# Kernel optimization log

Measured on AMD Instinct MI355X. Metric: run time of the kernel, lower is better.

Reference implementation:

```python
import jax, jax.numpy as jnp
import numpy as np

B, C, H, W = 4, 96, 56, 56
K0, K1, DIL, HID = 5, 7, 3, 4  # HID: ConvMlp(dim, expansion, drop) => hidden_features = int(mlp_ratio) = 4 (repo quirk)
EPS = 1e-5


def _conv(x, w, b, pad, dil=1, groups=1):
    y = jax.lax.conv_general_dilated(x, w, (1, 1), [(pad, pad), (pad, pad)],
                                     rhs_dilation=(dil, dil),
                                     dimension_numbers=('NCHW', 'OIHW', 'NCHW'),
                                     feature_group_count=groups)
    return y + b[None, :, None, None]


def _conv1x1(x, w, b):
    return jnp.einsum('bchw,oc->bohw', x, w) + b[None, :, None, None]


def _ln(x, g, b):
    # LayerNormProxy: LayerNorm over channel dim of NCHW
    mu = jnp.mean(x, axis=1, keepdims=True)
    v = jnp.var(x, axis=1, keepdims=True)
    return (x - mu) * jax.lax.rsqrt(v + EPS) * g[None, :, None, None] + b[None, :, None, None]


def _gelu(x):
    return jax.nn.gelu(x, approximate=False)  # torch nn.GELU default = exact erf


def _deform_dw(x, ow, ob, dw, db, k, dil, pad):
    # DeformConv2d wrapper: offsets from a same-geometry conv, then depthwise deformable conv.
    Bx, Cx, Hx, Wx = x.shape
    P = k * k
    off = _conv(x, ow, ob, pad, dil).reshape(Bx, P, 2, Hx, Wx)  # [B,P,(y,x),H,W]
    ky = (jnp.repeat(jnp.arange(k), k) * dil - pad).astype(x.dtype)  # row-major kernel grid
    kx = (jnp.tile(jnp.arange(k), k) * dil - pad).astype(x.dtype)
    py = jnp.arange(Hx, dtype=x.dtype)[None, None, :, None] + ky[None, :, None, None] + off[:, :, 0]
    px = jnp.arange(Wx, dtype=x.dtype)[None, None, None, :] + kx[None, :, None, None] + off[:, :, 1]
    y0 = jnp.floor(py)
    x0 = jnp.floor(px)
    wy = py - y0
    wx = px - x0
    xf = x.reshape(Bx, Cx, Hx * Wx)

    def corner(yi, xi):
        valid = (yi >= 0) & (yi < Hx) & (xi >= 0) & (xi < Wx)
        idx = (jnp.clip(yi, 0, Hx - 1).astype(jnp.int32) * Wx
               + jnp.clip(xi, 0, Wx - 1).astype(jnp.int32)).reshape(Bx, -1)
        g = jax.vmap(lambda a, i: jnp.take(a, i, axis=1))(xf, idx).reshape(Bx, Cx, P, Hx, Wx)
        return g * valid[:, None].astype(x.dtype)

    v = (corner(y0, x0) * ((1 - wy) * (1 - wx))[:, None]
         + corner(y0, x0 + 1) * ((1 - wy) * wx)[:, None]
         + corner(y0 + 1, x0) * (wy * (1 - wx))[:, None]
         + corner(y0 + 1, x0 + 1) * (wy * wx)[:, None])  # [B,C,P,H,W]
    return jnp.einsum('bcphw,cp->bchw', v, dw) + db[None, :, None, None]


def setup_inputs() -> dict:
    key = jax.random.key(0)
    ks = iter(jax.random.split(key, 32))

    def rn(shape, s=1.0):
        return jax.random.normal(next(ks), shape, jnp.float32) * s

    f32 = jnp.float32
    return {
        'x': rn((B, C, H, W)),
        'g1n': jnp.ones((C,), f32), 'b1n': jnp.zeros((C,), f32),
        'p1w': rn((C, C), 1 / np.sqrt(C)), 'p1b': jnp.zeros((C,), f32),
        'o0w': rn((2 * K0 * K0, C, K0, K0), 0.05 / np.sqrt(C * K0 * K0)), 'o0b': jnp.zeros((2 * K0 * K0,), f32),
        'd0w': rn((C, K0 * K0), 1 / np.sqrt(K0 * K0)), 'd0b': jnp.zeros((C,), f32),
        'o1w': rn((2 * K1 * K1, C, K1, K1), 0.05 / np.sqrt(C * K1 * K1)), 'o1b': jnp.zeros((2 * K1 * K1,), f32),
        'd1w': rn((C, K1 * K1), 1 / np.sqrt(K1 * K1)), 'd1b': jnp.zeros((C,), f32),
        'c1w': rn((C, C), 1 / np.sqrt(C)), 'c1b': jnp.zeros((C,), f32),
        'p2w': rn((C, C), 1 / np.sqrt(C)), 'p2b': jnp.zeros((C,), f32),
        'ls1': jnp.full((C,), 0.01, f32),
        'g2n': jnp.ones((C,), f32), 'b2n': jnp.zeros((C,), f32),
        'f1w': rn((HID, C), 1 / np.sqrt(C)), 'f1b': jnp.zeros((HID,), f32),
        'dww': rn((HID, 1, 3, 3), 1 / 3.0), 'dwb': jnp.zeros((HID,), f32),
        'f2w': rn((C, HID), 1 / np.sqrt(HID)), 'f2b': jnp.zeros((C,), f32),
        'ls2': jnp.full((C,), 0.01, f32),
    }


def reference(x, g1n, b1n, p1w, p1b, o0w, o0b, d0w, d0b, o1w, o1b, d1w, d1b,
              c1w, c1b, p2w, p2b, ls1, g2n, b2n, f1w, f1b, dww, dwb, f2w, f2b, ls2):
    # attention branch
    y = _ln(x, g1n, b1n)
    shortcut = y
    y = _gelu(_conv1x1(y, p1w, p1b))
    u = y
    a = _deform_dw(y, o0w, o0b, d0w, d0b, K0, 1, K0 // 2)
    a = _deform_dw(a, o1w, o1b, d1w, d1b, K1, DIL, (K1 // 2) * DIL)
    a = _conv1x1(a, c1w, c1b)
    y = _conv1x1(u * a, p2w, p2b) + shortcut
    y = ls1[None, :, None, None] * y
    x = x + y
    # MLP branch (note: norm2 is applied to the branch output y, as in the source)
    z = _ln(y, g2n, b2n)
    z = _conv1x1(z, f1w, f1b)
    z = _gelu(_conv(z, dww, dwb, 1, 1, HID))
    z = _conv1x1(z, f2w, f2b)
    x = x + ls2[None, :, None, None] * z
    return x
```

## Files before the change

kernel.cpp:

```cpp
#include <hip/hip_runtime.h>
#include <math.h>

namespace {

constexpr int Bc = 4, Cc = 96, Hc = 56, Wc = 56;
constexpr int HWc = Hc * Wc;
constexpr int Nc  = Bc * HWc;
constexpr float EPSc = 1e-5f;

typedef __attribute__((ext_vector_type(8))) short bf16x8;
typedef __attribute__((ext_vector_type(4))) float f32x4;
typedef __attribute__((ext_vector_type(4))) unsigned int u32x4;

__device__ __forceinline__ unsigned short f2bf(float f) {
  union { float f; unsigned u; } x; x.f = f;
  unsigned r = x.u + 0x7fffu + ((x.u >> 16) & 1u);
  return (unsigned short)(r >> 16);
}
__device__ __forceinline__ float bf2f(unsigned short u) {
  union { unsigned u; float f; } x; x.u = (unsigned)u << 16; return x.f;
}
__device__ __forceinline__ float gelu_exact(float x) {
  return 0.5f * x * (1.0f + erff(x * 0.7071067811865475f));
}

__global__ __launch_bounds__(256) void k_ln(const float* __restrict__ x,
                                            const float* __restrict__ g,
                                            const float* __restrict__ b,
                                            unsigned short* __restrict__ outN) {
  int pos = blockIdx.x * 256 + threadIdx.x;
  int bb = pos / HWc, hw = pos % HWc;
  const float* xb = x + (size_t)bb * Cc * HWc + hw;
  float s = 0.f, s2 = 0.f;
  for (int c = 0; c < Cc; ++c) { float v = xb[c * HWc]; s += v; s2 += v * v; }
  float mu  = s * (1.f / Cc);
  float var = fmaxf(s2 * (1.f / Cc) - mu * mu, 0.f);
  float rs  = rsqrtf(var + EPSc);
  unsigned short* ob = outN + (size_t)pos * Cc;
  for (int q = 0; q < 12; ++q) {
    unsigned short t8[8];
#pragma unroll
    for (int j = 0; j < 8; ++j) {
      int c = q * 8 + j;
      t8[j] = f2bf((xb[c * HWc] - mu) * rs * g[c] + b[c]);
    }
    *reinterpret_cast<bf16x8*>(ob + q * 8) = *reinterpret_cast<const bf16x8*>(t8);
  }
}

template <int K_, int MTILES, int P>
__global__ __launch_bounds__(256) void k_pack_w(const float* __restrict__ wsrc,
                                                unsigned short* __restrict__ wpk) {
  constexpr int TOTAL = K_ * K_ * 3 * MTILES * 512;
  int idx = blockIdx.x * 256 + threadIdx.x;
  if (idx >= TOTAL) return;
  int j    = idx & 7;
  int lane = (idx >> 3) & 63;
  int t    = idx >> 9;
  int mt   = t % MTILES;
  int step = t / MTILES;
  int o = mt * 16 + (lane & 15);
  int k = step * 32 + ((lane >> 4) & 3) * 8 + j;
  int p = k / Cc, c = k % Cc;
  float v = 0.f;
  if (o < P) v = wsrc[(((size_t)o * Cc + c) * K_ + p / K_) * K_ + (p % K_)];
  wpk[idx] = f2bf(v);
}

__global__ __launch_bounds__(256) void k_pack_dwt(const float* __restrict__ dwsrc,
                                                  float* __restrict__ dwt, int KK) {
  int idx = blockIdx.x * 256 + threadIdx.x;
  if (idx >= KK * Cc) return;
  int p = idx / Cc, c = idx % Cc;
  dwt[idx] = dwsrc[c * KK + p];
}

template <int GELU, int PADP, int WP>
__global__ __launch_bounds__(256) void k_pwg(const unsigned short* __restrict__ inN,
                                             const unsigned short* __restrict__ wpk,
                                             const float* __restrict__ bq,
                                             unsigned short* __restrict__ outPad) {
  int lane = threadIdx.x & 63;
  int wv = threadIdx.x >> 6;
  int ng = wv & 1, mg = wv >> 1;
  int n = blockIdx.x * 32 + ng * 16 + (lane & 15);
  int ko = ((lane >> 4) & 3) * 8;
  const unsigned short* ib = inN + (size_t)n * Cc + ko;
  const unsigned short* wl = wpk + (size_t)lane * 8;
  f32x4 acc[3];
#pragma unroll
  for (int m = 0; m < 3; ++m) acc[m] = (f32x4){0.f, 0.f, 0.f, 0.f};
#pragma unroll
  for (int ks = 0; ks < 3; ++ks) {
    bf16x8 bf = *reinterpret_cast<const bf16x8*>(ib + ks * 32);
#pragma unroll
    for (int m = 0; m < 3; ++m) {
      bf16x8 af = *reinterpret_cast<const bf16x8*>(wl + (size_t)(ks * 6 + mg * 3 + m) * 512);
      acc[m] = __builtin_amdgcn_mfma_f32_16x16x32_bf16(af, bf, acc[m], 0, 0, 0);
    }
  }
  int bb = n / HWc, hw = n % HWc;
  int h = hw / Wc, w = hw % Wc;
  unsigned short* ob = outPad + (((size_t)bb * (Hc + 2 * PADP) + h + PADP) * WP + w + PADP) * Cc;
  int orow = ((lane >> 4) & 3) * 4;
#pragma unroll
  for (int m = 0; m < 3; ++m) {
    int o0 = (mg * 3 + m) * 16 + orow;
    float4 bv = *reinterpret_cast<const float4*>(bq + o0);
    unsigned short t4[4];
#pragma unroll
    for (int j = 0; j < 4; ++j) {
      float r = acc[m][j] + ((const float*)&bv)[j];
      if (GELU) r = gelu_exact(r);
      t4[j] = f2bf(r);
    }
    *reinterpret_cast<uint2*>(ob + o0) = *reinterpret_cast<const uint2*>(t4);
  }
}

template <int UPADP, int UWP>
__global__ __launch_bounds__(256) void k_comb(const unsigned short* __restrict__ uPad,
                                              const unsigned short* __restrict__ An,
                                              const unsigned short* __restrict__ wpk,
                                              const float* __restrict__ bq,
                                              const unsigned short* __restrict__ ylnN,
                                              const float* __restrict__ ls1q,
                                              const float* __restrict__ x,
                                              float* __restrict__ out,
                                              unsigned short* __restrict__ y2N) {
  int lane = threadIdx.x & 63;
  int wv = threadIdx.x >> 6;
  int ng = wv & 1, mg = wv >> 1;
  int n = blockIdx.x * 32 + ng * 16 + (lane & 15);
  int ko = ((lane >> 4) & 3) * 8;
  int bb = n / HWc, hw = n % HWc;
  int h = hw / Wc, w = hw % Wc;
  const unsigned short* ub = uPad + (((size_t)bb * (Hc + 2 * UPADP) + h + UPADP) * UWP + w + UPADP) * Cc + ko;
  const unsigned short* ab = An + (size_t)n * Cc + ko;
  const unsigned short* wl = wpk + (size_t)lane * 8;
  f32x4 acc[3];
#pragma unroll
  for (int m = 0; m < 3; ++m) acc[m] = (f32x4){0.f, 0.f, 0.f, 0.f};
#pragma unroll
  for (int ks = 0; ks < 3; ++ks) {
    bf16x8 uv = *reinterpret_cast<const bf16x8*>(ub + ks * 32);
    bf16x8 av = *reinterpret_cast<const bf16x8*>(ab + ks * 32);
    union { bf16x8 v; unsigned short s[8]; } uu, aa, gg;
    uu.v = uv; aa.v = av;
#pragma unroll
    for (int j = 0; j < 8; ++j) gg.s[j] = f2bf(bf2f(uu.s[j]) * bf2f(aa.s[j]));
#pragma unroll
    for (int m = 0; m < 3; ++m) {
      bf16x8 af = *reinterpret_cast<const bf16x8*>(wl + (size_t)(ks * 6 + mg * 3 + m) * 512);
      acc[m] = __builtin_amdgcn_mfma_f32_16x16x32_bf16(af, gg.v, acc[m], 0, 0, 0);
    }
  }
  int orow = ((lane >> 4) & 3) * 4;
  const float* xb = x + (size_t)bb * Cc * HWc + hw;
  float* ob = out + (size_t)bb * Cc * HWc + hw;
#pragma unroll
  for (int m = 0; m < 3; ++m) {
    int o0 = (mg * 3 + m) * 16 + orow;
    float4 bv = *reinterpret_cast<const float4*>(bq + o0);
    float4 lv = *reinterpret_cast<const float4*>(ls1q + o0);
    uint2 yl = *reinterpret_cast<const uint2*>(ylnN + (size_t)n * Cc + o0);
    unsigned short yl4[4];
    *reinterpret_cast<uint2*>(yl4) = yl;
    unsigned short t4[4];
#pragma unroll
    for (int j = 0; j < 4; ++j) {
      float t = acc[m][j] + ((const float*)&bv)[j] + bf2f(yl4[j]);
      float y2 = ((const float*)&lv)[j] * t;
      t4[j] = f2bf(y2);
      ob[(size_t)(o0 + j) * HWc] = xb[(size_t)(o0 + j) * HWc] + y2;
    }
    *reinterpret_cast<uint2*>(y2N + (size_t)n * Cc + o0) = *reinterpret_cast<const uint2*>(t4);
  }
}

template <int K_, int DIL_, int MTILES, int P, int PADP, int WP, int PSTR, int SPLIT>
__global__ __launch_bounds__(256) void k_conv_mfma(const unsigned short* __restrict__ inp,
                                                   const unsigned short* __restrict__ wpk,
                                                   const float* __restrict__ bq,
                                                   float* __restrict__ dstT) {
  constexpr int KK = K_ * K_;
  constexpr int KKb = KK / SPLIT, KKr = KK % SPLIT;
  constexpr int HP = Hc + 2 * PADP;
  int lane = threadIdx.x & 63;
  int wv = threadIdx.x >> 6;
  int sp = blockIdx.y;
  int p0 = sp * KKb + min(sp, KKr);
  int pcnt = KKb + (sp < KKr ? 1 : 0);
  int n0 = blockIdx.x * 128 + wv * 32 + (lane & 15);
  int n1 = n0 + 16;
  int b0 = n0 / HWc, hw0 = n0 % HWc, h0 = hw0 / Wc, w0 = hw0 % Wc;
  int b1 = n1 / HWc, hw1 = n1 % HWc, h1 = hw1 / Wc, w1 = hw1 % Wc;
  int co = ((lane >> 4) & 3) * 8;
  const unsigned short* ib0 = inp + ((size_t)b0 * HP * WP + (size_t)h0 * WP + w0) * Cc + co;
  const unsigned short* ib1 = inp + ((size_t)b1 * HP * WP + (size_t)h1 * WP + w1) * Cc + co;
  const unsigned short* wl = wpk + (size_t)lane * 8;

  f32x4 acc[MTILES][2];
#pragma unroll
  for (int mt = 0; mt < MTILES; ++mt) {
    acc[mt][0] = (f32x4){0.f, 0.f, 0.f, 0.f};
    acc[mt][1] = (f32x4){0.f, 0.f, 0.f, 0.f};
  }

  for (int pi = 0; pi < pcnt; ++pi) {
    int p = p0 + pi;
    size_t toff = (size_t)((p / K_) * DIL_ * WP + (p % K_) * DIL_) * Cc;
    union { u32x4 u; bf16x8 v; } b0r[3], b1r[3];
#pragma unroll
    for (int cc = 0; cc < 3; ++cc) {
      b0r[cc].u = __builtin_nontemporal_load(reinterpret_cast<const u32x4*>(ib0 + toff + cc * 32));
      b1r[cc].u = __builtin_nontemporal_load(reinterpret_cast<const u32x4*>(ib1 + toff + cc * 32));
    }
#pragma unroll
    for (int cc = 0; cc < 3; ++cc) {
      const unsigned short* wa = wl + (size_t)(p * 3 + cc) * MTILES * 512;
#pragma unroll
      for (int mt = 0; mt < MTILES; ++mt) {
        bf16x8 A = *reinterpret_cast<const bf16x8*>(wa + (size_t)mt * 512);
        acc[mt][0] = __builtin_amdgcn_mfma_f32_16x16x32_bf16(A, b0r[cc].v, acc[mt][0], 0, 0, 0);
        acc[mt][1] = __builtin_amdgcn_mfma_f32_16x16x32_bf16(A, b1r[cc].v, acc[mt][1], 0, 0, 0);
      }
    }
  }

  float* dsp = dstT + (size_t)sp * Nc * PSTR;
  int orow = ((lane >> 4) & 3) * 4;
#pragma unroll
  for (int mt = 0; mt < MTILES; ++mt) {
#pragma unroll
    for (int nt = 0; nt < 2; ++nt) {
      float4 st;
#pragma unroll
      for (int j = 0; j < 4; ++j) {
        int o = mt * 16 + orow + j;
        float bias = (sp == 0 && o < P) ? bq[o] : 0.f;
        ((float*)&st)[j] = acc[mt][nt][j] + bias;
      }
      int n = nt ? n1 : n0;
      *reinterpret_cast<float4*>(dsp + (size_t)n * PSTR + mt * 16 + orow) = st;
    }
  }
}

template <int K_, int DIL_, int PAD_, int PSTR, int NSUM>
__global__ __launch_bounds__(256) void k_meta(const float* __restrict__ offT,
                                              uint4* __restrict__ meta) {
  constexpr int KK = K_ * K_;
  int idx = blockIdx.x * 256 + threadIdx.x;
  if (idx >= Nc * KK) return;
  int p = idx % KK, pos = idx / KK;
  int hw = pos % HWc;
  int h = hw / Wc, w = hw % Wc;
  const float* ob = offT + (size_t)pos * PSTR + 2 * p;
  float oy = ob[0], ox = ob[1];
#pragma unroll
  for (int q = 1; q < NSUM; ++q) {
    oy += ob[(size_t)q * Nc * PSTR];
    ox += ob[(size_t)q * Nc * PSTR + 1];
  }
  float py = (float)(h + (p / K_) * DIL_ - PAD_) + oy;
  float px = (float)(w + (p % K_) * DIL_ - PAD_) + ox;
  float y0f = floorf(py), x0f = floorf(px);
  float wy = py - y0f, wx = px - x0f;
  int y0 = (int)y0f, x0 = (int)x0f;
  int y1 = y0 + 1, x1 = x0 + 1;
  bool y0v = (unsigned)y0 < (unsigned)Hc, y1v = (unsigned)y1 < (unsigned)Hc;
  bool x0v = (unsigned)x0 < (unsigned)Wc, x1v = (unsigned)x1 < (unsigned)Wc;
  int y0c = min(max(y0, 0), Hc - 1), y1c = min(max(y1, 0), Hc - 1);
  int x0c = min(max(x0, 0), Wc - 1), x1c = min(max(x1, 0), Wc - 1);
  float w00 = (y0v && x0v) ? (1.f - wy) * (1.f - wx) : 0.f;
  float w01 = (y0v && x1v) ? (1.f - wy) * wx : 0.f;
  float w10 = (y1v && x0v) ? wy * (1.f - wx) : 0.f;
  float w11 = (y1v && x1v) ? wy * wx : 0.f;
  uint4 m;
  m.x = (unsigned)(y0c | (y1c << 6) | (x0c << 12) | (x1c << 18));
  m.y = 0;
  m.z = (unsigned)f2bf(w00) | ((unsigned)f2bf(w01) << 16);
  m.w = (unsigned)f2bf(w10) | ((unsigned)f2bf(w11) << 16);
  meta[idx] = m;
}

template <int K_, int IPADP, int IWP, int OPADP, int OWP>
__global__ __launch_bounds__(256) void k_deform3(const unsigned short* __restrict__ srcT,
                                                 const uint4* __restrict__ meta,
                                                 const float* __restrict__ dwt,
                                                 const float* __restrict__ dbq,
                                                 unsigned short* __restrict__ dstPad) {
  constexpr int KK = K_ * K_;
  constexpr int IHP = Hc + 2 * IPADP;
  __shared__ float sdwt[KK * Cc];
  for (int i = threadIdx.x; i < KK * Cc; i += 256) sdwt[i] = dwt[i];
  __syncthreads();

  int tid = blockIdx.x * 256 + threadIdx.x;
  int cg = tid % 24;
  int pos = tid / 24;
  int c = cg * 4;
  int bb = pos / HWc, hw = pos % HWc;
  int h = hw / Wc, w = hw % Wc;
  const unsigned short* sb = srcT + ((size_t)bb * IHP * IWP + IPADP * IWP + IPADP) * Cc + c;
  const uint4* mt = meta + (size_t)pos * KK;
  float ac0 = 0.f, ac1 = 0.f, ac2 = 0.f, ac3 = 0.f;

  constexpr int BT = 4;
  int p = 0;
  for (; p + BT <= KK; p += BT) {
    uint4 m[BT];
#pragma unroll
    for (int i = 0; i < BT; ++i) m[i] = mt[p + i];
    uint2 v[BT][4];
#pragma unroll
    for (int i = 0; i < BT; ++i) {
      unsigned ix = m[i].x;
      int y0 = (int)(ix & 63u), y1 = (int)((ix >> 6) & 63u);
      int x0 = (int)((ix >> 12) & 63u), x1 = (int)((ix >> 18) & 63u);
      const unsigned short* r0 = sb + (size_t)(y0 * IWP) * Cc;
      const unsigned short* r1 = sb + (size_t)(y1 * IWP) * Cc;
      v[i][0] = *reinterpret_cast<const uint2*>(r0 + x0 * Cc);
      v[i][1] = *reinterpret_cast<const uint2*>(r0 + x1 * Cc);
      v[i][2] = *reinterpret_cast<const uint2*>(r1 + x0 * Cc);
      v[i][3] = *reinterpret_cast<const uint2*>(r1 + x1 * Cc);
    }
#pragma unroll
    for (int i = 0; i < BT; ++i) {
      float w00 = bf2f((unsigned short)(m[i].z & 0xffffu));
      float w01 = bf2f((unsigned short)(m[i].z >> 16));
      float w10 = bf2f((unsigned short)(m[i].w & 0xffffu));
      float w11 = bf2f((unsigned short)(m[i].w >> 16));
      float4 d = *reinterpret_cast<const float4*>(&sdwt[(p + i) * Cc + c]);
#pragma unroll
      for (int j = 0; j < 2; ++j) {
        unsigned u00 = ((const unsigned*)&v[i][0])[j];
        unsigned u01 = ((const unsigned*)&v[i][1])[j];
        unsigned u10 = ((const unsigned*)&v[i][2])[j];
        unsigned u11 = ((const unsigned*)&v[i][3])[j];
        union { unsigned u; float f; } a0_, b0_, a1_, b1_, a2_, b2_, a3_, b3_;
        a0_.u = u00 << 16; b0_.u = u00 & 0xffff0000u;
        a1_.u = u01 << 16; b1_.u = u01 & 0xffff0000u;
        a2_.u = u10 << 16; b2_.u = u10 & 0xffff0000u;
        a3_.u = u11 << 16; b3_.u = u11 & 0xffff0000u;
        float lo = w00 * a0_.f + w01 * a1_.f + w10 * a2_.f + w11 * a3_.f;
        float hi = w00 * b0_.f + w01 * b1_.f + w10 * b2_.f + w11 * b3_.f;
        if (j == 0) { ac0 += lo * d.x; ac1 += hi * d.y; }
        else        { ac2 += lo * d.z; ac3 += hi * d.w; }
      }
    }
  }
  {
    uint4 m = mt[p];
    unsigned ix = m.x;
    int y0 = (int)(ix & 63u), y1 = (int)((ix >> 6) & 63u);
    int x0 = (int)((ix >> 12) & 63u), x1 = (int)((ix >> 18) & 63u);
    const unsigned short* r0 = sb + (size_t)(y0 * IWP) * Cc;
    const unsigned short* r1 = sb + (size_t)(y1 * IWP) * Cc;
    uint2 v0 = *reinterpret_cast<const uint2*>(r0 + x0 * Cc);
    uint2 v1 = *reinterpret_cast<const uint2*>(r0 + x1 * Cc);
    uint2 v2 = *reinterpret_cast<const uint2*>(r1 + x0 * Cc);
    uint2 v3 = *reinterpret_cast<const uint2*>(r1 + x1 * Cc);
    float w00 = bf2f((unsigned short)(m.z & 0xffffu));
    float w01 = bf2f((unsigned short)(m.z >> 16));
    float w10 = bf2f((unsigned short)(m.w & 0xffffu));
    float w11 = bf2f((unsigned short)(m.w >> 16));
    float4 d = *reinterpret_cast<const float4*>(&sdwt[p * Cc + c]);
#pragma unroll
    for (int j = 0; j < 2; ++j) {
      unsigned u00 = ((const unsigned*)&v0)[j];
      unsigned u01 = ((const unsigned*)&v1)[j];
      unsigned u10 = ((const unsigned*)&v2)[j];
      unsigned u11 = ((const unsigned*)&v3)[j];
      union { unsigned u; float f; } a0_, b0_, a1_, b1_, a2_, b2_, a3_, b3_;
      a0_.u = u00 << 16; b0_.u = u00 & 0xffff0000u;
      a1_.u = u01 << 16; b1_.u = u01 & 0xffff0000u;
      a2_.u = u10 << 16; b2_.u = u10 & 0xffff0000u;
      a3_.u = u11 << 16; b3_.u = u11 & 0xffff0000u;
      float lo = w00 * a0_.f + w01 * a1_.f + w10 * a2_.f + w11 * a3_.f;
      float hi = w00 * b0_.f + w01 * b1_.f + w10 * b2_.f + w11 * b3_.f;
      if (j == 0) { ac0 += lo * d.x; ac1 += hi * d.y; }
      else        { ac2 += lo * d.z; ac3 += hi * d.w; }
    }
  }

  unsigned short t4[4] = {f2bf(ac0 + dbq[c]), f2bf(ac1 + dbq[c + 1]),
                          f2bf(ac2 + dbq[c + 2]), f2bf(ac3 + dbq[c + 3])};
  unsigned short* tb = dstPad + (((size_t)bb * (Hc + 2 * OPADP) + h + OPADP) * OWP + w + OPADP) * Cc + c;
  *reinterpret_cast<uint2*>(tb) = *reinterpret_cast<const uint2*>(t4);
}

__global__ __launch_bounds__(256) void k_mlp1(const unsigned short* __restrict__ y2N,
                                              const float* __restrict__ g,
                                              const float* __restrict__ b,
                                              const float* __restrict__ f1wq,
                                              const float* __restrict__ f1bq,
                                              float* __restrict__ z4) {
  int pos = blockIdx.x * 256 + threadIdx.x;
  int bb = pos / HWc, hw = pos % HWc;
  const unsigned short* yb = y2N + (size_t)pos * Cc;
  float vv[96];
  float s = 0.f, s2 = 0.f;
#pragma unroll
  for (int q = 0; q < 12; ++q) {
    bf16x8 t = *reinterpret_cast<const bf16x8*>(yb + q * 8);
    union { bf16x8 v; unsigned short s[8]; } u; u.v = t;
#pragma unroll
    for (int j = 0; j < 8; ++j) {
      float f = bf2f(u.s[j]);
      vv[q * 8 + j] = f; s += f; s2 += f * f;
    }
  }
  float mu  = s * (1.f / Cc);
  float var = fmaxf(s2 * (1.f / Cc) - mu * mu, 0.f);
  float rs  = rsqrtf(var + EPSc);
  float a0 = 0.f, a1 = 0.f, a2 = 0.f, a3 = 0.f;
#pragma unroll
  for (int c = 0; c < 96; ++c) {
    float t = (vv[c] - mu) * rs * g[c] + b[c];
    a0 += t * f1wq[0 * Cc + c];
    a1 += t * f1wq[1 * Cc + c];
    a2 += t * f1wq[2 * Cc + c];
    a3 += t * f1wq[3 * Cc + c];
  }
  float* zb = z4 + (size_t)bb * 4 * HWc + hw;
  zb[0 * HWc] = a0 + f1bq[0];
  zb[1 * HWc] = a1 + f1bq[1];
  zb[2 * HWc] = a2 + f1bq[2];
  zb[3 * HWc] = a3 + f1bq[3];
}

__global__ __launch_bounds__(256) void k_mlp_dw(const float* __restrict__ z4,
                                                const float* __restrict__ dwwq,
                                                const float* __restrict__ dwbq,
                                                float* __restrict__ z4b) {
  int tid = blockIdx.x * 256 + threadIdx.x;
  int hw = tid % HWc;
  int bj = tid / HWc;
  int j = bj % 4;
  int h = hw / Wc, w = hw % Wc;
  const float* zb = z4 + (size_t)bj * HWc;
  float s = 0.f;
#pragma unroll
  for (int ky = 0; ky < 3; ++ky) {
    int y = h + ky - 1;
    if ((unsigned)y >= (unsigned)Hc) continue;
#pragma unroll
    for (int kx = 0; kx < 3; ++kx) {
      int x = w + kx - 1;
      if ((unsigned)x >= (unsigned)Wc) continue;
      s += zb[y * Wc + x] * dwwq[j * 9 + ky * 3 + kx];
    }
  }
  z4b[tid] = gelu_exact(s + dwbq[j]);
}

__global__ __launch_bounds__(256) void k_mlp2(const float* __restrict__ z4b,
                                              const float* __restrict__ f2wq,
                                              const float* __restrict__ f2bq,
                                              const float* __restrict__ ls2q,
                                              float* __restrict__ out) {
  int pos = blockIdx.x * 256 + threadIdx.x;
  int bb = pos / HWc, hw = pos % HWc;
  const float* zb = z4b + (size_t)bb * 4 * HWc + hw;
  float z0 = zb[0 * HWc], z1 = zb[1 * HWc], z2 = zb[2 * HWc], z3 = zb[3 * HWc];
  float* ob = out + (size_t)bb * Cc * HWc + hw;
  for (int o = 0; o < Cc; ++o) {
    float s = f2bq[o] + z0 * f2wq[o * 4 + 0] + z1 * f2wq[o * 4 + 1]
                      + z2 * f2wq[o * 4 + 2] + z3 * f2wq[o * 4 + 3];
    ob[o * HWc] += ls2q[o] * s;
  }
}

}

extern "C" void kernel_launch(void* const* d_in, const int* in_sizes, int n_in,
                              void* d_out, int out_size, void* d_ws, size_t ws_size,
                              hipStream_t stream) {
  (void)in_sizes; (void)n_in; (void)out_size; (void)ws_size;
  const float* x   = (const float*)d_in[0];
  const float* g1n = (const float*)d_in[1];
  const float* b1n = (const float*)d_in[2];
  const float* p1w = (const float*)d_in[3];
  const float* p1b = (const float*)d_in[4];
  const float* o0w = (const float*)d_in[5];
  const float* o0b = (const float*)d_in[6];
  const float* d0w = (const float*)d_in[7];
  const float* d0b = (const float*)d_in[8];
  const float* o1w = (const float*)d_in[9];
  const float* o1b = (const float*)d_in[10];
  const float* d1w = (const float*)d_in[11];
  const float* d1b = (const float*)d_in[12];
  const float* c1w = (const float*)d_in[13];
  const float* c1b = (const float*)d_in[14];
  const float* p2w = (const float*)d_in[15];
  const float* p2b = (const float*)d_in[16];
  const float* ls1 = (const float*)d_in[17];
  const float* g2n = (const float*)d_in[18];
  const float* b2n = (const float*)d_in[19];
  const float* f1w = (const float*)d_in[20];
  const float* f1b = (const float*)d_in[21];
  const float* dww = (const float*)d_in[22];
  const float* dwb = (const float*)d_in[23];
  const float* f2w = (const float*)d_in[24];
  const float* f2b = (const float*)d_in[25];
  const float* ls2 = (const float*)d_in[26];
  float* out = (float*)d_out;
  float* ws  = (float*)d_ws;

  float* off0t = ws;                                  size_t o_ = (size_t)2 * Nc * 64;
  float* off1t = ws + o_;                             o_ += (size_t)4 * Nc * 112;
  float* z4    = ws + o_;                             o_ += (size_t)Bc * 4 * HWc;
  float* z4b   = ws + o_;                             o_ += (size_t)Bc * 4 * HWc;
  float* dwt0  = ws + o_;                             o_ += 25 * Cc;
  float* dwt1  = ws + o_;                             o_ += 49 * Cc + 4;
  o_ = (o_ + 3) & ~(size_t)3;
  uint4* metaM0 = (uint4*)(ws + o_);                  o_ += (size_t)Nc * 25 * 4;
  uint4* metaM1 = (uint4*)(ws + o_);                  o_ += (size_t)Nc * 49 * 4;
  unsigned short* yln_n  = (unsigned short*)(ws + o_); o_ += (size_t)Nc * Cc / 2;
  unsigned short* a1_n   = (unsigned short*)(ws + o_); o_ += (size_t)Nc * Cc / 2;
  unsigned short* A_n    = (unsigned short*)(ws + o_); o_ += (size_t)Nc * Cc / 2;
  unsigned short* y2_n   = (unsigned short*)(ws + o_); o_ += (size_t)Nc * Cc / 2;
  unsigned short* u_pad  = (unsigned short*)(ws + o_); o_ += (size_t)Bc * 60 * 60 * Cc / 2;
  unsigned short* a0_pad = (unsigned short*)(ws + o_); o_ += (size_t)Bc * 74 * 74 * Cc / 2;
  unsigned short* wpk0   = (unsigned short*)(ws + o_); o_ += (size_t)25 * 3 * 4 * 512 / 2;
  unsigned short* wpk1   = (unsigned short*)(ws + o_); o_ += (size_t)49 * 3 * 7 * 512 / 2;
  unsigned short* wpkp1  = (unsigned short*)(ws + o_); o_ += (size_t)3 * 6 * 512 / 2;
  unsigned short* wpkc1  = (unsigned short*)(ws + o_); o_ += (size_t)3 * 6 * 512 / 2;
  unsigned short* wpkp2  = (unsigned short*)(ws + o_); o_ += (size_t)3 * 6 * 512 / 2;

  dim3 b256(256, 1, 1);

  hipMemsetAsync(u_pad, 0, (size_t)Bc * 60 * 60 * Cc * sizeof(unsigned short), stream);
  hipMemsetAsync(a0_pad, 0, (size_t)Bc * 74 * 74 * Cc * sizeof(unsigned short), stream);
  hipLaunchKernelGGL((k_pack_w<5, 4, 50>), dim3((25 * 3 * 4 * 512 + 255) / 256), b256, 0, stream, o0w, wpk0);
  hipLaunchKernelGGL((k_pack_w<7, 7, 98>), dim3((49 * 3 * 7 * 512 + 255) / 256), b256, 0, stream, o1w, wpk1);
  hipLaunchKernelGGL((k_pack_w<1, 6, 96>), dim3((3 * 6 * 512 + 255) / 256), b256, 0, stream, p1w, wpkp1);
  hipLaunchKernelGGL((k_pack_w<1, 6, 96>), dim3((3 * 6 * 512 + 255) / 256), b256, 0, stream, c1w, wpkc1);
  hipLaunchKernelGGL((k_pack_w<1, 6, 96>), dim3((3 * 6 * 512 + 255) / 256), b256, 0, stream, p2w, wpkp2);
  hipLaunchKernelGGL(k_pack_dwt, dim3((25 * Cc + 255) / 256), b256, 0, stream, d0w, dwt0, 25);
  hipLaunchKernelGGL(k_pack_dwt, dim3((49 * Cc + 255) / 256), b256, 0, stream, d1w, dwt1, 49);

  hipLaunchKernelGGL(k_ln, dim3(Nc / 256), b256, 0, stream, x, g1n, b1n, yln_n);
  hipLaunchKernelGGL((k_pwg<1, 2, 60>), dim3(Nc / 32), b256, 0, stream, yln_n, wpkp1, p1b, u_pad);
  hipLaunchKernelGGL((k_conv_mfma<5, 1, 4, 50, 2, 60, 64, 2>), dim3(Nc / 128, 2), b256, 0, stream,
                     u_pad, wpk0, o0b, off0t);
  hipLaunchKernelGGL((k_meta<5, 1, 2, 64, 2>), dim3((Nc * 25 + 255) / 256), b256, 0, stream,
                     off0t, metaM0);
  hipLaunchKernelGGL((k_deform3<5, 2, 60, 9, 74>), dim3(Nc * 24 / 256), b256, 0, stream,
                     u_pad, metaM0, dwt0, d0b, a0_pad);
  hipLaunchKernelGGL((k_conv_mfma<7, 3, 7, 98, 9, 74, 112, 4>), dim3(Nc / 128, 4), b256, 0, stream,
                     a0_pad, wpk1, o1b, off1t);
  hipLaunchKernelGGL((k_meta<7, 3, 9, 112, 4>), dim3((Nc * 49 + 255) / 256), b256, 0, stream,
                     off1t, metaM1);
  hipLaunchKernelGGL((k_deform3<7, 9, 74, 0, 56>), dim3(Nc * 24 / 256), b256, 0, stream,
                     a0_pad, metaM1, dwt1, d1b, a1_n);
  hipLaunchKernelGGL((k_pwg<0, 0, 56>), dim3(Nc / 32), b256, 0, stream, a1_n, wpkc1, c1b, A_n);
  hipLaunchKernelGGL((k_comb<2, 60>), dim3(Nc / 32), b256, 0, stream,
                     u_pad, A_n, wpkp2, p2b, yln_n, ls1, x, out, y2_n);
  hipLaunchKernelGGL(k_mlp1, dim3(Nc / 256), b256, 0, stream, y2_n, g2n, b2n, f1w, f1b, z4);
  hipLaunchKernelGGL(k_mlp_dw, dim3(Nc * 4 / 256), b256, 0, stream, z4, dww, dwb, z4b);
  hipLaunchKernelGGL(k_mlp2, dim3(Nc / 256), b256, 0, stream, z4b, f2w, f2b, ls2, out);
}
```

Measured before the change: 249.3 us.

## Stage offset-conv weights and input taps in double-buffered LDS

Replaces the direct-global-load offset convolution with a version that cooperatively loads each tap's packed weights and the block's 128 input pixel rows into padded, double-buffered shared memory. The next tap is prefetched into registers while MFMAs run on the current buffer. Weights are now read once per block instead of once per wave. The second conv's K-split drops from 4 to 2, which halves the partial-offset buffer and the summation in the meta kernel but also halves that kernel's grid parallelism. The added __syncthreads per tap and the large LDS footprint may lower occupancy.

```diff
diff --git a/kernel.cpp b/kernel.cpp
--- a/kernel.cpp
+++ b/kernel.cpp
@@ -179,26 +179,67 @@
 }
 
 template <int K_, int DIL_, int MTILES, int P, int PADP, int WP, int PSTR, int SPLIT>
-__global__ __launch_bounds__(256) void k_conv_mfma(const unsigned short* __restrict__ inp,
-                                                   const unsigned short* __restrict__ wpk,
-                                                   const float* __restrict__ bq,
-                                                   float* __restrict__ dstT) {
+__global__ __launch_bounds__(256) void k_conv_lds(const unsigned short* __restrict__ inp,
+                                                  const unsigned short* __restrict__ wpk,
+                                                  const float* __restrict__ bq,
+                                                  float* __restrict__ dstT) {
   constexpr int KK = K_ * K_;
   constexpr int KKb = KK / SPLIT, KKr = KK % SPLIT;
   constexpr int HP = Hc + 2 * PADP;
-  int lane = threadIdx.x & 63;
-  int wv = threadIdx.x >> 6;
+  constexpr int ASH = 3 * MTILES * 512;
+  constexpr int BSTR = 104;
+  constexpr int BSH = 128 * BSTR;
+  constexpr int ACH = ASH / 8;
+  constexpr int BCH = 128 * 13;
+  constexpr int TOT = ACH + BCH;
+  constexpr int ITERS = (TOT + 255) / 256;
+  __shared__ unsigned short smem[2][ASH + BSH];
+
+  int tid = threadIdx.x;
+  int lane = tid & 63;
+  int wv = tid >> 6;
   int sp = blockIdx.y;
   int p0 = sp * KKb + min(sp, KKr);
   int pcnt = KKb + (sp < KKr ? 1 : 0);
-  int n0 = blockIdx.x * 128 + wv * 32 + (lane & 15);
-  int n1 = n0 + 16;
-  int b0 = n0 / HWc, hw0 = n0 % HWc, h0 = hw0 / Wc, w0 = hw0 % Wc;
-  int b1 = n1 / HWc, hw1 = n1 % HWc, h1 = hw1 / Wc, w1 = hw1 % Wc;
-  int co = ((lane >> 4) & 3) * 8;
-  const unsigned short* ib0 = inp + ((size_t)b0 * HP * WP + (size_t)h0 * WP + w0) * Cc + co;
-  const unsigned short* ib1 = inp + ((size_t)b1 * HP * WP + (size_t)h1 * WP + w1) * Cc + co;
-  const unsigned short* wl = wpk + (size_t)lane * 8;
+  int n0 = blockIdx.x * 128;
+
+  const unsigned short* gbase[ITERS];
+  int ldsOff[ITERS];
+  int isA[ITERS];
+#pragma unroll
+  for (int it = 0; it < ITERS; ++it) {
+    int c = tid + it * 256;
+    if (c < ACH) {
+      gbase[it] = wpk + (size_t)c * 8;
+      ldsOff[it] = c * 8;
+      isA[it] = 1;
+    } else if (c < TOT) {
+      int bc = c - ACH;
+      int pl = bc / 13, sub = bc % 13;
+      int subc = min(sub, 11);
+      int n = n0 + pl;
+      int b = n / HWc, hw = n % HWc, h = hw / Wc, w = hw % Wc;
+      gbase[it] = inp + ((size_t)b * HP * WP + (size_t)h * WP + w) * Cc + subc * 8;
+      ldsOff[it] = ASH + pl * BSTR + sub * 8;
+      isA[it] = 0;
+    } else {
+      gbase[it] = nullptr;
+      ldsOff[it] = 0;
+      isA[it] = 0;
+    }
+  }
+
+  u32x4 reg[ITERS];
+  {
+    size_t ta = (size_t)p0 * ASH;
+    size_t tb = (size_t)((p0 / K_) * DIL_ * WP + (p0 % K_) * DIL_) * Cc;
+#pragma unroll
+    for (int it = 0; it < ITERS; ++it)
+      if (gbase[it]) reg[it] = *reinterpret_cast<const u32x4*>(gbase[it] + (isA[it] ? ta : tb));
+#pragma unroll
+    for (int it = 0; it < ITERS; ++it)
+      if (gbase[it]) *reinterpret_cast<u32x4*>(&smem[0][ldsOff[it]]) = reg[it];
+  }
 
   f32x4 acc[MTILES][2];
 #pragma unroll
@@ -207,25 +248,39 @@
     acc[mt][1] = (f32x4){0.f, 0.f, 0.f, 0.f};
   }
 
+  int posl0 = wv * 32 + (lane & 15);
+  int co = ((lane >> 4) & 3) * 8;
+  int cur = 0;
   for (int pi = 0; pi < pcnt; ++pi) {
-    int p = p0 + pi;
-    size_t toff = (size_t)((p / K_) * DIL_ * WP + (p % K_) * DIL_) * Cc;
-    union { u32x4 u; bf16x8 v; } b0r[3], b1r[3];
+    __syncthreads();
+    bool more = (pi + 1 < pcnt);
+    if (more) {
+      int pn = p0 + pi + 1;
+      size_t ta = (size_t)pn * ASH;
+      size_t tb = (size_t)((pn / K_) * DIL_ * WP + (pn % K_) * DIL_) * Cc;
+#pragma unroll
+      for (int it = 0; it < ITERS; ++it)
+        if (gbase[it]) reg[it] = *reinterpret_cast<const u32x4*>(gbase[it] + (isA[it] ? ta : tb));
+    }
+    const unsigned short* sA = smem[cur];
+    const unsigned short* sB = smem[cur] + ASH;
 #pragma unroll
     for (int cc = 0; cc < 3; ++cc) {
-      b0r[cc].u = __builtin_nontemporal_load(reinterpret_cast<const u32x4*>(ib0 + toff + cc * 32));
-      b1r[cc].u = __builtin_nontemporal_load(reinterpret_cast<const u32x4*>(ib1 + toff + cc * 32));
-    }
-#pragma unroll
-    for (int cc = 0; cc < 3; ++cc) {
-      const unsigned short* wa = wl + (size_t)(p * 3 + cc) * MTILES * 512;
+      bf16x8 B0 = *reinterpret_cast<const bf16x8*>(sB + posl0 * BSTR + co + cc * 32);
+      bf16x8 B1 = *reinterpret_cast<const bf16x8*>(sB + (posl0 + 16) * BSTR + co + cc * 32);
 #pragma unroll
       for (int mt = 0; mt < MTILES; ++mt) {
-        bf16x8 A = *reinterpret_cast<const bf16x8*>(wa + (size_t)mt * 512);
-        acc[mt][0] = __builtin_amdgcn_mfma_f32_16x16x32_bf16(A, b0r[cc].v, acc[mt][0], 0, 0, 0);
-        acc[mt][1] = __builtin_amdgcn_mfma_f32_16x16x32_bf16(A, b1r[cc].v, acc[mt][1], 0, 0, 0);
+        bf16x8 A = *reinterpret_cast<const bf16x8*>(sA + (cc * MTILES + mt) * 512 + lane * 8);
+        acc[mt][0] = __builtin_amdgcn_mfma_f32_16x16x32_bf16(A, B0, acc[mt][0], 0, 0, 0);
+        acc[mt][1] = __builtin_amdgcn_mfma_f32_16x16x32_bf16(A, B1, acc[mt][1], 0, 0, 0);
       }
     }
+    if (more) {
+#pragma unroll
+      for (int it = 0; it < ITERS; ++it)
+        if (gbase[it]) *reinterpret_cast<u32x4*>(&smem[cur ^ 1][ldsOff[it]]) = reg[it];
+    }
+    cur ^= 1;
   }
 
   float* dsp = dstT + (size_t)sp * Nc * PSTR;
@@ -241,7 +296,7 @@
         float bias = (sp == 0 && o < P) ? bq[o] : 0.f;
         ((float*)&st)[j] = acc[mt][nt][j] + bias;
       }
-      int n = nt ? n1 : n0;
+      int n = n0 + posl0 + nt * 16;
       *reinterpret_cast<float4*>(dsp + (size_t)n * PSTR + mt * 16 + orow) = st;
     }
   }
@@ -510,7 +565,7 @@
   float* ws  = (float*)d_ws;
 
   float* off0t = ws;                                  size_t o_ = (size_t)2 * Nc * 64;
-  float* off1t = ws + o_;                             o_ += (size_t)4 * Nc * 112;
+  float* off1t = ws + o_;                             o_ += (size_t)2 * Nc * 112;
   float* z4    = ws + o_;                             o_ += (size_t)Bc * 4 * HWc;
   float* z4b   = ws + o_;                             o_ += (size_t)Bc * 4 * HWc;
   float* dwt0  = ws + o_;                             o_ += 25 * Cc;
@@ -544,15 +599,15 @@
 
   hipLaunchKernelGGL(k_ln, dim3(Nc / 256), b256, 0, stream, x, g1n, b1n, yln_n);
   hipLaunchKernelGGL((k_pwg<1, 2, 60>), dim3(Nc / 32), b256, 0, stream, yln_n, wpkp1, p1b, u_pad);
-  hipLaunchKernelGGL((k_conv_mfma<5, 1, 4, 50, 2, 60, 64, 2>), dim3(Nc / 128, 2), b256, 0, stream,
+  hipLaunchKernelGGL((k_conv_lds<5, 1, 4, 50, 2, 60, 64, 2>), dim3(Nc / 128, 2), b256, 0, stream,
                      u_pad, wpk0, o0b, off0t);
   hipLaunchKernelGGL((k_meta<5, 1, 2, 64, 2>), dim3((Nc * 25 + 255) / 256), b256, 0, stream,
                      off0t, metaM0);
   hipLaunchKernelGGL((k_deform3<5, 2, 60, 9, 74>), dim3(Nc * 24 / 256), b256, 0, stream,
                      u_pad, metaM0, dwt0, d0b, a0_pad);
-  hipLaunchKernelGGL((k_conv_mfma<7, 3, 7, 98, 9, 74, 112, 4>), dim3(Nc / 128, 4), b256, 0, stream,
+  hipLaunchKernelGGL((k_conv_lds<7, 3, 7, 98, 9, 74, 112, 2>), dim3(Nc / 128, 2), b256, 0, stream,
                      a0_pad, wpk1, o1b, off1t);
-  hipLaunchKernelGGL((k_meta<7, 3, 9, 112, 4>), dim3((Nc * 49 + 255) / 256), b256, 0, stream,
+  hipLaunchKernelGGL((k_meta<7, 3, 9, 112, 2>), dim3((Nc * 49 + 255) / 256), b256, 0, stream,
                      off1t, metaM1);
   hipLaunchKernelGGL((k_deform3<7, 9, 74, 0, 56>), dim3(Nc * 24 / 256), b256, 0, stream,
                      a0_pad, metaM1, dwt1, d1b, a1_n);
```

Result: slower. 268.0 us (+7.5%).
